# Optimization experiments

Hardware: AMD Instinct MI355X
Metric: run time of the kernel (lower is better)

The kernel has to match this reference:

```python
import jax, jax.numpy as jnp
import numpy as np

NEG_INF = -1e9  # matches masked_fill value in the torch source


def setup_inputs() -> dict:
    key0 = jax.random.key(0)
    kq, kk, kv, km = jax.random.split(key0, 4)
    B, H, S, D = 2, 12, 2048, 64
    query = jax.random.normal(kq, (B, H, S, D), dtype=jnp.float32)
    key = jax.random.normal(kk, (B, H, S, D), dtype=jnp.float32)
    value = jax.random.normal(kv, (B, H, S, D), dtype=jnp.float32)
    mask = jax.random.randint(km, (B, S, S), 0, 2, dtype=jnp.int32)
    return {"query": query, "key": key, "value": value, "mask": mask}


def reference(query, key, value, mask):
    # query/key/value: [B, H, S, D]; mask: [B, S, S] (0 = masked out)
    d = key.shape[-1]
    scale = 1.0 / np.sqrt(d).astype(np.float32)
    # attn scores: [B, H, Sq, Sk]
    attn = jnp.einsum("bhqd,bhkd->bhqk", query * scale, key)
    m = mask[:, None, :, :]  # broadcast over heads, mirrors mask.unsqueeze(1)
    attn = jnp.where(m == 0, jnp.float32(NEG_INF), attn)
    attn = jax.nn.softmax(attn, axis=-1)
    # dropout_ratio = 0.0 -> identity
    out = jnp.einsum("bhqk,bhkd->bhqd", attn, value)
    return out
```

## Files before the change

### kernel.cpp

```cpp
#include <hip/hip_runtime.h>

#define SQ 2048
#define DH 64
#define NH 12
#define NBH 24

typedef __attribute__((ext_vector_type(8))) short short8;
typedef __attribute__((ext_vector_type(16))) float f32x16;

union U8 { uint4 u; short8 s; };

__device__ __forceinline__ unsigned short f2bf(float x) {
  union { float f; unsigned u; } v; v.f = x;
  return (unsigned short)((v.u + 0x7FFFu + ((v.u >> 16) & 1u)) >> 16);
}

__device__ __forceinline__ unsigned pk2(float a, float b) {
  unsigned ua = __builtin_bit_cast(unsigned, a) + 0x8000u;
  unsigned ub = __builtin_bit_cast(unsigned, b) + 0x8000u;
  return __builtin_amdgcn_perm(ub, ua, 0x07060302);
}

__device__ __forceinline__ void gload_lds16(const void* g, void* l) {
  __builtin_amdgcn_global_load_lds(
      (const __attribute__((address_space(1))) unsigned*)g,
      (__attribute__((address_space(3))) unsigned*)l, 16, 0, 0);
}

__device__ __forceinline__ int sw23(int x) {
  return (x & 19) | ((x & 4) << 1) | ((x & 8) >> 1);
}

__global__ __launch_bounds__(256) void prep_all(
    const float* __restrict__ Q, const float* __restrict__ K,
    const float* __restrict__ V, const int* __restrict__ M,
    unsigned short* __restrict__ Qb, unsigned short* __restrict__ Kb,
    unsigned short* __restrict__ Vt, unsigned* __restrict__ mbits) {
  const int bid = blockIdx.x, tid = threadIdx.x;
  if (bid < 3072) {
    int i = bid * 256 + tid;
    float4 q = ((const float4*)Q)[i];
    float4 k = ((const float4*)K)[i];
    const float sc = 0.125f * 1.44269504f;
    ushort4 qo, ko;
    qo.x = f2bf(q.x * sc); qo.y = f2bf(q.y * sc);
    qo.z = f2bf(q.z * sc); qo.w = f2bf(q.w * sc);
    ko.x = f2bf(k.x); ko.y = f2bf(k.y); ko.z = f2bf(k.z); ko.w = f2bf(k.w);
    ((ushort4*)Qb)[i] = qo;
    ((ushort4*)Kb)[i] = ko;
  } else if (bid < 3840) {
    __shared__ float T[64 * 65];
    int bx = bid - 3072;
    int bh = bx >> 5, st = bx & 31;
    int s0 = st * 64;
    int c4 = (tid & 15) * 4, r0 = tid >> 4;
#pragma unroll
    for (int it = 0; it < 4; ++it) {
      int r = r0 + 16 * it;
      float4 v = *(const float4*)(V + ((size_t)(bh * SQ + s0 + r)) * DH + c4);
      T[r * 65 + c4 + 0] = v.x; T[r * 65 + c4 + 1] = v.y;
      T[r * 65 + c4 + 2] = v.z; T[r * 65 + c4 + 3] = v.w;
    }
    __syncthreads();
#pragma unroll
    for (int it = 0; it < 2; ++it) {
      int cc = tid + 256 * it;
      int d = cc >> 3, c8 = (cc & 7) * 8;
      short8 o;
#pragma unroll
      for (int j = 0; j < 8; ++j) o[j] = (short)f2bf(T[(c8 + j) * 65 + d]);
      *(short8*)(Vt + ((size_t)(bh * 64 + d)) * SQ + s0 + c8) = o;
    }
  } else {
    int w = tid >> 6, lane = tid & 63;
    int row = (bid - 3840) * 4 + w;
    const int* mrow = M + (size_t)row * SQ;
    unsigned long long out = 0;
#pragma unroll
    for (int j = 0; j < 32; ++j) {
      int mv = mrow[j * 64 + lane];
      unsigned long long bits = __ballot(mv != 0);
      if (lane == j) out = bits;
    }
    if (lane < 32)
      ((unsigned long long*)mbits)[(size_t)row * 32 + lane] = out;
  }
}

__global__ __launch_bounds__(256, 3) void attn_kernel(
    const unsigned short* __restrict__ Qb, const unsigned short* __restrict__ Kb,
    const unsigned short* __restrict__ Vt, const unsigned* __restrict__ mbits,
    float* __restrict__ O0, float* __restrict__ O1, float* __restrict__ Lp) {
  __shared__ uint4 FIFO[2][16][64];

  const int bx = blockIdx.x;
  const int bh = bx % NBH;
  const int rest = bx / NBH;
  const int qt = rest & 15, ks = rest >> 4;
  const int b = bh / NH;
  const int tid = threadIdx.x;
  const int lane = tid & 63, w = tid >> 6;
  const int n = lane & 31, h = lane >> 5;
  const int qrow = qt * 128 + w * 32 + n;
  const int k0 = ks * (SQ / 2);

  short8 qf[4];
#pragma unroll
  for (int s = 0; s < 4; ++s)
    qf[s] = *(const short8*)(Qb + ((size_t)(bh * SQ + qrow)) * DH + 16 * s + 8 * h);

  const unsigned short* gp[4];
  if (w < 2) {
#pragma unroll
    for (int j = 0; j < 4; ++j) {
      int c = 4 * w + j;
      int row = k0 + 32 * (c >> 2) + sw23(n);
      gp[j] = Kb + ((size_t)bh * SQ + row) * DH + 16 * (c & 3) + 8 * h;
    }
  } else {
#pragma unroll
    for (int j = 0; j < 4; ++j) {
      int cc = 4 * (w - 2) + j;
      gp[j] = Vt + ((size_t)bh * DH + 32 * (cc >> 2) + n) * SQ + k0 + 16 * (cc & 3) + 8 * h;
    }
  }
  const int gstride = (w < 2) ? 64 * DH : 64;
  const int chunk0 = w * 4;

  const unsigned long long* mp =
      (const unsigned long long*)mbits + ((size_t)b * SQ + qrow) * 32 + (k0 >> 6);

  short8 ones;
#pragma unroll
  for (int j = 0; j < 8; ++j) ones[j] = (short)0x3F80;

  f32x16 acc0 = {0,0,0,0,0,0,0,0,0,0,0,0,0,0,0,0};
  f32x16 acc1 = {0,0,0,0,0,0,0,0,0,0,0,0,0,0,0,0};
  f32x16 sumac = {0,0,0,0,0,0,0,0,0,0,0,0,0,0,0,0};

#pragma unroll
  for (int j = 0; j < 4; ++j) {
    gload_lds16(gp[j], &FIFO[0][chunk0 + j][0]);
    gp[j] += gstride;
  }
  __syncthreads();

  for (int nt = 0; nt < 16; ++nt) {
    const int cur = nt & 1;
    if (nt < 15) {
#pragma unroll
      for (int j = 0; j < 4; ++j) {
        gload_lds16(gp[j], &FIFO[1 - cur][chunk0 + j][0]);
        gp[j] += gstride;
      }
    }
    unsigned long long mg = *mp; ++mp;

    short8 pb[2][2];
#pragma unroll
    for (int u = 0; u < 2; ++u) {
      f32x16 st = {0,0,0,0,0,0,0,0,0,0,0,0,0,0,0,0};
#pragma unroll
      for (int s = 0; s < 4; ++s) {
        U8 kf; kf.u = FIFO[cur][4 * u + s][lane];
        st = __builtin_amdgcn_mfma_f32_32x32x16_bf16(kf.s, qf[s], st, 0, 0, 0);
      }
      unsigned blo = (unsigned)(mg >> (8 * (4 * u + h))) & 0xFFu;
      unsigned bhi = (unsigned)(mg >> (8 * (4 * u + 2 + h))) & 0xFFu;
      float p[16];
#pragma unroll
      for (int j = 0; j < 16; ++j) {
        float e = __builtin_amdgcn_exp2f(st[j]);
        unsigned byt = (j < 8) ? blo : bhi;
        p[j] = ((byt >> (j & 7)) & 1u) ? e : 0.f;
      }
      U8 x0, x1;
      x0.u = (uint4){pk2(p[0], p[1]), pk2(p[2], p[3]), pk2(p[4], p[5]), pk2(p[6], p[7])};
      x1.u = (uint4){pk2(p[8], p[9]), pk2(p[10], p[11]), pk2(p[12], p[13]), pk2(p[14], p[15])};
      pb[u][0] = x0.s;
      pb[u][1] = x1.s;
    }

#pragma unroll
    for (int t = 0; t < 4; ++t) {
      short8 pf = pb[t >> 1][t & 1];
      sumac = __builtin_amdgcn_mfma_f32_32x32x16_bf16(ones, pf, sumac, 0, 0, 0);
      U8 v0; v0.u = FIFO[cur][8 + t][lane];
      acc0 = __builtin_amdgcn_mfma_f32_32x32x16_bf16(v0.s, pf, acc0, 0, 0, 0);
      U8 v1; v1.u = FIFO[cur][12 + t][lane];
      acc1 = __builtin_amdgcn_mfma_f32_32x32x16_bf16(v1.s, pf, acc1, 0, 0, 0);
    }

    __syncthreads();
  }

  float* op = (ks ? O1 : O0) + ((size_t)(bh * SQ + qrow)) * DH;
#pragma unroll
  for (int dt = 0; dt < 2; ++dt) {
    f32x16 A = dt ? acc1 : acc0;
#pragma unroll
    for (int a = 0; a < 4; ++a) {
      float4 o = {A[4 * a], A[4 * a + 1], A[4 * a + 2], A[4 * a + 3]};
      *(float4*)(op + 32 * dt + 8 * a + 4 * h) = o;
    }
  }
  if (lane < 32) Lp[(size_t)ks * NBH * SQ + bh * SQ + qrow] = sumac[0];
}

__global__ __launch_bounds__(256) void combine(float* __restrict__ Out,
                                               const float* __restrict__ O1,
                                               const float* __restrict__ Lp) {
  int i = blockIdx.x * 256 + threadIdx.x;
  float4 a = ((const float4*)Out)[i];
  float4 bb = ((const float4*)O1)[i];
  int q = i >> 4;
  float inv = __builtin_amdgcn_rcpf(Lp[q] + Lp[NBH * SQ + q]);
  float4 o = {(a.x + bb.x) * inv, (a.y + bb.y) * inv,
              (a.z + bb.z) * inv, (a.w + bb.w) * inv};
  ((float4*)Out)[i] = o;
}

extern "C" void kernel_launch(void* const* d_in, const int* in_sizes, int n_in,
                              void* d_out, int out_size, void* d_ws, size_t ws_size,
                              hipStream_t stream) {
  const float* Q = (const float*)d_in[0];
  const float* K = (const float*)d_in[1];
  const float* V = (const float*)d_in[2];
  const int*   M = (const int*)d_in[3];
  float* Out = (float*)d_out;

  size_t NB = (size_t)NBH * SQ * DH;
  unsigned short* Qb = (unsigned short*)d_ws;
  unsigned short* Kb = Qb + NB;
  unsigned short* Vt = Kb + NB;
  unsigned* mbits = (unsigned*)(Vt + NB);
  float* O1 = (float*)(mbits + (size_t)2 * SQ * 64);
  float* Lp = O1 + NB;

  prep_all<<<4864, 256, 0, stream>>>(Q, K, V, M, Qb, Kb, Vt, mbits);
  attn_kernel<<<NBH * 16 * 2, 256, 0, stream>>>(Qb, Kb, Vt, mbits, Out, O1, Lp);
  combine<<<(int)(NB / 4 / 256), 256, 0, stream>>>(Out, O1, Lp);
}
```

Baseline: 157.3 us.

## Triple-buffer K/V LDS FIFO with partial vmcnt waits and prefetched mask

Grows the LDS staging ring from two to three stages so global-to-LDS loads run two tiles ahead of compute. The full __syncthreads is replaced by a partial s_waitcnt vmcnt(4) plus a raw s_barrier, so only the next tile's loads must land. The mask word for the next tile is also loaded one iteration early. This hides global load latency behind MFMA work, at the cost of 50% more LDS per block, which may reduce occupancy. It also relies on hand-written waitcnt values matching the compiler's memory-op counts, including the mask loads.

```diff
diff --git a/kernel.cpp b/kernel.cpp
--- a/kernel.cpp
+++ b/kernel.cpp
@@ -91,7 +91,7 @@
     const unsigned short* __restrict__ Qb, const unsigned short* __restrict__ Kb,
     const unsigned short* __restrict__ Vt, const unsigned* __restrict__ mbits,
     float* __restrict__ O0, float* __restrict__ O1, float* __restrict__ Lp) {
-  __shared__ uint4 FIFO[2][16][64];
+  __shared__ uint4 FIFO[3][16][64];
 
   const int bx = blockIdx.x;
   const int bh = bx % NBH;
@@ -138,23 +138,32 @@
   f32x16 acc1 = {0,0,0,0,0,0,0,0,0,0,0,0,0,0,0,0};
   f32x16 sumac = {0,0,0,0,0,0,0,0,0,0,0,0,0,0,0,0};
 
+  unsigned long long mg_cur = *mp; ++mp;
 #pragma unroll
   for (int j = 0; j < 4; ++j) {
     gload_lds16(gp[j], &FIFO[0][chunk0 + j][0]);
     gp[j] += gstride;
   }
-  __syncthreads();
-
+#pragma unroll
+  for (int j = 0; j < 4; ++j) {
+    gload_lds16(gp[j], &FIFO[1][chunk0 + j][0]);
+    gp[j] += gstride;
+  }
+  asm volatile("s_waitcnt vmcnt(4)" ::: "memory");
+  asm volatile("s_barrier" ::: "memory");
+
+  int cur = 0;
   for (int nt = 0; nt < 16; ++nt) {
-    const int cur = nt & 1;
-    if (nt < 15) {
+    unsigned long long mg_next = 0;
+    if (nt < 15) { mg_next = *mp; ++mp; }
+    if (nt < 14) {
+      int pf = cur + 2; if (pf >= 3) pf -= 3;
 #pragma unroll
       for (int j = 0; j < 4; ++j) {
-        gload_lds16(gp[j], &FIFO[1 - cur][chunk0 + j][0]);
+        gload_lds16(gp[j], &FIFO[pf][chunk0 + j][0]);
         gp[j] += gstride;
       }
     }
-    unsigned long long mg = *mp; ++mp;
 
     short8 pb[2][2];
 #pragma unroll
@@ -165,8 +174,8 @@
         U8 kf; kf.u = FIFO[cur][4 * u + s][lane];
         st = __builtin_amdgcn_mfma_f32_32x32x16_bf16(kf.s, qf[s], st, 0, 0, 0);
       }
-      unsigned blo = (unsigned)(mg >> (8 * (4 * u + h))) & 0xFFu;
-      unsigned bhi = (unsigned)(mg >> (8 * (4 * u + 2 + h))) & 0xFFu;
+      unsigned blo = (unsigned)(mg_cur >> (8 * (4 * u + h))) & 0xFFu;
+      unsigned bhi = (unsigned)(mg_cur >> (8 * (4 * u + 2 + h))) & 0xFFu;
       float p[16];
 #pragma unroll
       for (int j = 0; j < 16; ++j) {
@@ -183,15 +192,20 @@
 
 #pragma unroll
     for (int t = 0; t < 4; ++t) {
-      short8 pf = pb[t >> 1][t & 1];
-      sumac = __builtin_amdgcn_mfma_f32_32x32x16_bf16(ones, pf, sumac, 0, 0, 0);
+      short8 pf8 = pb[t >> 1][t & 1];
+      sumac = __builtin_amdgcn_mfma_f32_32x32x16_bf16(ones, pf8, sumac, 0, 0, 0);
       U8 v0; v0.u = FIFO[cur][8 + t][lane];
-      acc0 = __builtin_amdgcn_mfma_f32_32x32x16_bf16(v0.s, pf, acc0, 0, 0, 0);
+      acc0 = __builtin_amdgcn_mfma_f32_32x32x16_bf16(v0.s, pf8, acc0, 0, 0, 0);
       U8 v1; v1.u = FIFO[cur][12 + t][lane];
-      acc1 = __builtin_amdgcn_mfma_f32_32x32x16_bf16(v1.s, pf, acc1, 0, 0, 0);
-    }
-
-    __syncthreads();
+      acc1 = __builtin_amdgcn_mfma_f32_32x32x16_bf16(v1.s, pf8, acc1, 0, 0, 0);
+    }
+
+    if (nt < 14)       asm volatile("s_waitcnt vmcnt(4)" ::: "memory");
+    else if (nt == 14) asm volatile("s_waitcnt vmcnt(0)" ::: "memory");
+    if (nt < 15)       asm volatile("s_barrier" ::: "memory");
+
+    mg_cur = mg_next;
+    cur += 1; if (cur >= 3) cur -= 3;
   }
 
   float* op = (ks ? O1 : O0) + ((size_t)(bh * SQ + qrow)) * DH;
```

New measurement: 177.4 us. 1.13x slower.
